# Optimization experiments

Hardware: AMD Instinct MI355X
Metric: run time of the kernel (lower is better)

Reference implementation:

```python
import jax, jax.numpy as jnp
import numpy as np

B, Q, D, H, DH = 4, 1024, 1024, 16, 64  # batch, qlen(=klen), d_model, n_head, d_head
SCALE = 1.0 / np.sqrt(DH)
_INF = -1e30
LN_EPS = 1e-5


def setup_inputs() -> dict:
    key = jax.random.key(0)
    ks = jax.random.split(key, 10)
    w = jax.random.normal(ks[0], (B, Q, D), jnp.float32)
    r = jax.random.normal(ks[1], (Q, D), jnp.float32)
    r_w_bias = jax.random.normal(ks[2], (H, DH), jnp.float32) * 0.02
    r_r_bias = jax.random.normal(ks[3], (H, DH), jnp.float32) * 0.02
    # causal mask: nonzero = attend (torch masks where attn_mask == 0)
    attn_mask = jnp.tile(jnp.tril(jnp.ones((Q, Q), bool))[None], (B, 1, 1))
    # linear weights stored torch-style: (out_features, in_features), no bias
    Wq = jax.random.normal(ks[4], (H * DH, D), jnp.float32) * SCALE
    Wk = jax.random.normal(ks[5], (H * DH, D), jnp.float32) * SCALE
    Wv = jax.random.normal(ks[6], (H * DH, D), jnp.float32) * SCALE
    Wo = jax.random.normal(ks[7], (D, H * DH), jnp.float32) * SCALE
    Wr = jax.random.normal(ks[8], (H * DH, D), jnp.float32) * (1.0 / np.sqrt(H * DH))
    ln_gamma = jnp.ones((D,), jnp.float32)
    ln_beta = jnp.zeros((D,), jnp.float32)
    return {"w": w, "r": r, "r_w_bias": r_w_bias, "r_r_bias": r_r_bias,
            "attn_mask": attn_mask, "Wq": Wq, "Wk": Wk, "Wv": Wv, "Wr": Wr,
            "Wo": Wo, "ln_gamma": ln_gamma, "ln_beta": ln_beta}


def _layer_norm(x, gamma, beta):
    mu = jnp.mean(x, axis=-1, keepdims=True)
    var = jnp.mean(jnp.square(x - mu), axis=-1, keepdims=True)
    return (x - mu) * jax.lax.rsqrt(var + LN_EPS) * gamma + beta


def _rel_shift(x):
    # faithful to this repo: pad one zero column on key axis then drop first
    # column -> left-shift along j with trailing zeros (no reshape trick)
    return jnp.concatenate([x[:, :, 1:, :], jnp.zeros_like(x[:, :, :1, :])], axis=2)


def reference(w, r, r_w_bias, r_r_bias, attn_mask, Wq, Wk, Wv, Wr, Wo, ln_gamma, ln_beta):
    bsz, qlen, _ = w.shape
    klen = qlen  # no mems
    r_head_k = (r @ Wr.T).reshape(klen, H, DH)          # [K,H,Dh]
    w_head_q = (w @ Wq.T).reshape(bsz, qlen, H, DH)     # [B,Q,H,Dh]
    w_head_k = (w @ Wk.T).reshape(bsz, klen, H, DH)
    w_head_v = (w @ Wv.T).reshape(bsz, klen, H, DH)
    AC = jnp.einsum('bind,bjnd->bijn', w_head_q + r_w_bias, w_head_k)
    BD = jnp.einsum('bind,jnd->bijn', w_head_q + r_r_bias, r_head_k)
    BD = _rel_shift(BD)
    attn_score = (AC + BD) * SCALE                      # [B,Q,K,H]
    attn_score = jnp.where(attn_mask[..., None], attn_score, _INF)
    attn_prob = jax.nn.softmax(attn_score, axis=2)
    attn_vec = jnp.einsum('bijn,bjnd->bind', attn_prob, w_head_v)
    attn_vec = attn_vec.reshape(bsz, qlen, H * DH)
    attn_out = attn_vec @ Wo.T
    return _layer_norm(w + attn_out, ln_gamma, ln_beta)
```

## Files before the change

kernel.cpp:

```cpp
#include <hip/hip_runtime.h>
#include <math.h>

typedef _Float16 F16;
typedef __attribute__((ext_vector_type(8))) _Float16 f16x8;
typedef __attribute__((ext_vector_type(4))) float f32x4;

__global__ __launch_bounds__(256) void cvt_kernel(const float* __restrict__ src,
                                                  F16* __restrict__ dst, int n4) {
  int i = blockIdx.x * 256 + threadIdx.x;
  if (i >= n4) return;
  float4 v = reinterpret_cast<const float4*>(src)[i];
  union { F16 h[4]; uint2 u; } pk;
  pk.h[0] = (F16)v.x; pk.h[1] = (F16)v.y; pk.h[2] = (F16)v.z; pk.h[3] = (F16)v.w;
  reinterpret_cast<uint2*>(dst)[i] = pk.u;
}

__global__ void fill_kernel(F16* __restrict__ Kt) {
  int id = blockIdx.x * 256 + threadIdx.x;
  int b = id >> 10, h = (id >> 6) & 15, d = id & 63;
  Kt[(((size_t)(b * 16 + h)) * 1024 + 1023) * 128 + 64 + d] = (F16)0.f;
}

template <int MODE>
__global__ __launch_bounds__(256) void gemm_bt(const F16* __restrict__ A,
                                               const F16* __restrict__ W,
                                               const float* __restrict__ bias1,
                                               const float* __restrict__ bias2,
                                               F16* __restrict__ outp,
                                               float* __restrict__ outf,
                                               const float* __restrict__ addsrc) {
  const int tid = threadIdx.x;
  const int lane = tid & 63, wid = tid >> 6;
  const int wm = wid >> 1, wn = wid & 1;
  const int l15 = lane & 15, g = lane >> 4, hi8 = g * 8;
  const int m0 = blockIdx.x * 128, n0 = blockIdx.y * 128;

  __shared__ __align__(16) F16 As[128][72];
  __shared__ __align__(16) F16 Bs[128][72];

  f32x4 acc[4][4] = {};

  for (int k0 = 0; k0 < 1024; k0 += 64) {
#pragma unroll
    for (int j = 0; j < 4; ++j) {
      int chunk = tid + j * 256;
      int r = chunk >> 3, cc = (chunk & 7) * 8;
      *(uint4*)&As[r][cc] = *(const uint4*)&A[(size_t)(m0 + r) * 1024 + k0 + cc];
      *(uint4*)&Bs[r][cc] = *(const uint4*)&W[(size_t)(n0 + r) * 1024 + k0 + cc];
    }
    __syncthreads();
#pragma unroll
    for (int kk = 0; kk < 2; ++kk) {
      f16x8 a[4], b[4];
#pragma unroll
      for (int m = 0; m < 4; ++m) a[m] = *(const f16x8*)&As[wm * 64 + m * 16 + l15][kk * 32 + hi8];
#pragma unroll
      for (int n = 0; n < 4; ++n) b[n] = *(const f16x8*)&Bs[wn * 64 + n * 16 + l15][kk * 32 + hi8];
#pragma unroll
      for (int m = 0; m < 4; ++m)
#pragma unroll
        for (int n = 0; n < 4; ++n)
          acc[m][n] = __builtin_amdgcn_mfma_f32_16x16x32_f16(a[m], b[n], acc[m][n], 0, 0, 0);
    }
    __syncthreads();
  }

#pragma unroll
  for (int m = 0; m < 4; ++m)
#pragma unroll
    for (int n = 0; n < 4; ++n)
#pragma unroll
      for (int i = 0; i < 4; ++i) {
        int row = m0 + wm * 64 + m * 16 + g * 4 + i;
        int col = n0 + wn * 64 + n * 16 + l15;
        float v = acc[m][n][i];
        if (MODE == 0) {
          int b = row >> 10, q = row & 1023, h = col >> 6, d = col & 63;
          size_t base = (((size_t)(b * 16 + h)) * 1024 + q) * 128;
          outp[base + d]      = (F16)((v + bias1[col]) * 0.125f);
          outp[base + 64 + d] = (F16)((v + bias2[col]) * 0.125f);
        } else if (MODE == 1) {
          int b = row >> 10, q = row & 1023, h = col >> 6, d = col & 63;
          outp[(((size_t)(b * 16 + h)) * 1024 + q) * 128 + d] = (F16)v;
        } else if (MODE == 2) {
          int b = row >> 10, q = row & 1023, h = col >> 6, d = col & 63;
          outp[(((size_t)(b * 16 + h)) * 64 + d) * 1024 + q] = (F16)v;
        } else if (MODE == 3) {
          if (row > 0) {
            int h = col >> 6, d = col & 63;
#pragma unroll
            for (int b2 = 0; b2 < 4; ++b2)
              outp[(((size_t)(b2 * 16 + h)) * 1024 + (row - 1)) * 128 + 64 + d] = (F16)v;
          }
        } else {
          outf[(size_t)row * 1024 + col] = v + addsrc[(size_t)row * 1024 + col];
        }
      }
}

__global__ __launch_bounds__(256) void attn_kernel(const F16* __restrict__ Qt,
                                                   const F16* __restrict__ Kt,
                                                   const F16* __restrict__ Vt,
                                                   F16* __restrict__ av) {
  const int qb = blockIdx.x, h = blockIdx.y, b = blockIdx.z;
  const int tid = threadIdx.x, lane = tid & 63, w = tid >> 6;
  const int l15 = lane & 15, g = lane >> 4, hi8 = g * 8;
  const size_t bh = (size_t)(b * 16 + h);
  const F16* Qb = Qt + bh * 1024 * 128;
  const F16* Kb = Kt + bh * 1024 * 128;
  const F16* Vb = Vt + bh * 64 * 1024;

  __shared__ __align__(16) F16 Ks[64][136];
  __shared__ __align__(16) F16 Vs[64][72];
  __shared__ __align__(16) F16 Ps[4][16][72];

  f16x8 qf[4];
  const int qrow = qb * 64 + w * 16 + l15;
#pragma unroll
  for (int t = 0; t < 4; ++t)
    qf[t] = *(const f16x8*)&Qb[(size_t)qrow * 128 + t * 32 + hi8];

  f32x4 accO[4] = {};
  float mi[4], li[4];
#pragma unroll
  for (int i = 0; i < 4; ++i) { mi[i] = -INFINITY; li[i] = 0.f; }

  for (int kt = 0; kt <= qb; ++kt) {
#pragma unroll
    for (int j = 0; j < 4; ++j) {
      int chunk = tid + j * 256;
      int r = chunk >> 4, cc = (chunk & 15) * 8;
      *(uint4*)&Ks[r][cc] = *(const uint4*)&Kb[(size_t)(kt * 64 + r) * 128 + cc];
    }
#pragma unroll
    for (int j = 0; j < 2; ++j) {
      int chunk = tid + j * 256;
      int r = chunk >> 3, cc = (chunk & 7) * 8;
      *(uint4*)&Vs[r][cc] = *(const uint4*)&Vb[(size_t)r * 1024 + kt * 64 + cc];
    }
    __syncthreads();

    f32x4 s[4] = {};
#pragma unroll
    for (int st = 0; st < 4; ++st)
#pragma unroll
      for (int t = 0; t < 4; ++t) {
        f16x8 kf = *(const f16x8*)&Ks[st * 16 + l15][t * 32 + hi8];
        s[st] = __builtin_amdgcn_mfma_f32_16x16x32_f16(qf[t], kf, s[st], 0, 0, 0);
      }

    if (kt == qb) {
#pragma unroll
      for (int st = 0; st < 4; ++st)
#pragma unroll
        for (int i = 0; i < 4; ++i) {
          int row = qb * 64 + w * 16 + g * 4 + i;
          int col = kt * 64 + st * 16 + l15;
          if (col > row) s[st][i] = -1e30f;
        }
    }

#pragma unroll
    for (int i = 0; i < 4; ++i) {
      float v = fmaxf(fmaxf(s[0][i], s[1][i]), fmaxf(s[2][i], s[3][i]));
      v = fmaxf(v, __shfl_xor(v, 1));
      v = fmaxf(v, __shfl_xor(v, 2));
      v = fmaxf(v, __shfl_xor(v, 4));
      v = fmaxf(v, __shfl_xor(v, 8));
      float mnew = fmaxf(mi[i], v);
      float sum = 0.f;
#pragma unroll
      for (int st = 0; st < 4; ++st) {
        float p = __expf(s[st][i] - mnew);
        sum += p;
        Ps[w][g * 4 + i][st * 16 + l15] = (F16)p;
      }
      sum += __shfl_xor(sum, 1);
      sum += __shfl_xor(sum, 2);
      sum += __shfl_xor(sum, 4);
      sum += __shfl_xor(sum, 8);
      float alpha = __expf(mi[i] - mnew);
      li[i] = li[i] * alpha + sum;
      mi[i] = mnew;
#pragma unroll
      for (int n = 0; n < 4; ++n) accO[n][i] *= alpha;
    }

#pragma unroll
    for (int t2 = 0; t2 < 2; ++t2) {
      f16x8 pa = *(const f16x8*)&Ps[w][l15][t2 * 32 + hi8];
#pragma unroll
      for (int n = 0; n < 4; ++n) {
        f16x8 vb = *(const f16x8*)&Vs[n * 16 + l15][t2 * 32 + hi8];
        accO[n] = __builtin_amdgcn_mfma_f32_16x16x32_f16(pa, vb, accO[n], 0, 0, 0);
      }
    }
    __syncthreads();
  }

#pragma unroll
  for (int n = 0; n < 4; ++n)
#pragma unroll
    for (int i = 0; i < 4; ++i) {
      int row = qb * 64 + w * 16 + g * 4 + i;
      av[((size_t)b * 1024 + row) * 1024 + h * 64 + n * 16 + l15] =
          (F16)(accO[n][i] / li[i]);
    }
}

__global__ __launch_bounds__(256) void ln_kernel(const float* __restrict__ x,
                                                 const float* __restrict__ gamma,
                                                 const float* __restrict__ beta,
                                                 float* __restrict__ out) {
  const int row = blockIdx.x;
  const int t = threadIdx.x;
  const float* xr = x + (size_t)row * 1024;
  float4 v = reinterpret_cast<const float4*>(xr)[t];
  float s = v.x + v.y + v.z + v.w;
  float s2 = v.x * v.x + v.y * v.y + v.z * v.z + v.w * v.w;
  for (int off = 32; off; off >>= 1) {
    s += __shfl_down(s, off);
    s2 += __shfl_down(s2, off);
  }
  __shared__ float ps[4], ps2[4];
  int wid = t >> 6, ln = t & 63;
  if (ln == 0) { ps[wid] = s; ps2[wid] = s2; }
  __syncthreads();
  if (t == 0) {
    float a = 0, c = 0;
    for (int i = 0; i < 4; ++i) { a += ps[i]; c += ps2[i]; }
    ps[0] = a; ps2[0] = c;
  }
  __syncthreads();
  float mean = ps[0] * (1.f / 1024.f);
  float var = ps2[0] * (1.f / 1024.f) - mean * mean;
  float rstd = rsqrtf(var + 1e-5f);
  float4 gm = reinterpret_cast<const float4*>(gamma)[t];
  float4 bt = reinterpret_cast<const float4*>(beta)[t];
  float4 o;
  o.x = (v.x - mean) * rstd * gm.x + bt.x;
  o.y = (v.y - mean) * rstd * gm.y + bt.y;
  o.z = (v.z - mean) * rstd * gm.z + bt.z;
  o.w = (v.w - mean) * rstd * gm.w + bt.w;
  reinterpret_cast<float4*>(out + (size_t)row * 1024)[t] = o;
}

extern "C" void kernel_launch(void* const* d_in, const int* in_sizes, int n_in,
                              void* d_out, int out_size, void* d_ws, size_t ws_size,
                              hipStream_t stream) {
  const float* w = (const float*)d_in[0];
  const float* r = (const float*)d_in[1];
  const float* rwb = (const float*)d_in[2];
  const float* rrb = (const float*)d_in[3];
  const float* Wq = (const float*)d_in[5];
  const float* Wk = (const float*)d_in[6];
  const float* Wv = (const float*)d_in[7];
  const float* Wr = (const float*)d_in[8];
  const float* Wo = (const float*)d_in[9];
  const float* gamma = (const float*)d_in[10];
  const float* beta = (const float*)d_in[11];
  float* out = (float*)d_out;

  char* ws = (char*)d_ws;
  size_t off = 0;
  F16* w_bf = (F16*)(ws + off); off += (size_t)4096 * 1024 * 2;
  F16* r_bf = (F16*)(ws + off); off += (size_t)1024 * 1024 * 2;
  F16* wq_bf = (F16*)(ws + off); off += (size_t)1024 * 1024 * 2;
  F16* wk_bf = (F16*)(ws + off); off += (size_t)1024 * 1024 * 2;
  F16* wv_bf = (F16*)(ws + off); off += (size_t)1024 * 1024 * 2;
  F16* wr_bf = (F16*)(ws + off); off += (size_t)1024 * 1024 * 2;
  F16* wo_bf = (F16*)(ws + off); off += (size_t)1024 * 1024 * 2;
  F16* Qt = (F16*)(ws + off); off += (size_t)4 * 16 * 1024 * 128 * 2;
  F16* Kt = (F16*)(ws + off); off += (size_t)4 * 16 * 1024 * 128 * 2;
  F16* Vt = (F16*)(ws + off); off += (size_t)4 * 16 * 64 * 1024 * 2;
  F16* av = (F16*)(ws + off); off += (size_t)4096 * 1024 * 2;
  float* tmp = (float*)(ws + off); off += (size_t)4096 * 1024 * 4;

  cvt_kernel<<<4096, 256, 0, stream>>>(w, w_bf, 1048576);
  cvt_kernel<<<1024, 256, 0, stream>>>(r, r_bf, 262144);
  cvt_kernel<<<1024, 256, 0, stream>>>(Wq, wq_bf, 262144);
  cvt_kernel<<<1024, 256, 0, stream>>>(Wk, wk_bf, 262144);
  cvt_kernel<<<1024, 256, 0, stream>>>(Wv, wv_bf, 262144);
  cvt_kernel<<<1024, 256, 0, stream>>>(Wr, wr_bf, 262144);
  cvt_kernel<<<1024, 256, 0, stream>>>(Wo, wo_bf, 262144);
  fill_kernel<<<16, 256, 0, stream>>>(Kt);

  gemm_bt<0><<<dim3(32, 8), 256, 0, stream>>>(w_bf, wq_bf, rwb, rrb, Qt, nullptr, nullptr);
  gemm_bt<1><<<dim3(32, 8), 256, 0, stream>>>(w_bf, wk_bf, nullptr, nullptr, Kt, nullptr, nullptr);
  gemm_bt<2><<<dim3(32, 8), 256, 0, stream>>>(w_bf, wv_bf, nullptr, nullptr, Vt, nullptr, nullptr);
  gemm_bt<3><<<dim3(8, 8), 256, 0, stream>>>(r_bf, wr_bf, nullptr, nullptr, Kt, nullptr, nullptr);

  attn_kernel<<<dim3(16, 16, 4), 256, 0, stream>>>(Qt, Kt, Vt, av);

  gemm_bt<4><<<dim3(32, 8), 256, 0, stream>>>(av, wo_bf, nullptr, nullptr, nullptr, tmp, w);
  ln_kernel<<<4096, 256, 0, stream>>>(tmp, gamma, beta, out);
}
```

Measured before the change: 353.9 us.

## Fuse QKV projection GEMMs, pair causal attention tiles, double-buffer and swizzle K/V LDS

The Q, K and V weights are packed into one 3072-column matrix so a single GEMM launch with a widened grid produces all three outputs, each with its own epilogue layout. The attention kernel now has each block process a pair of query tiles (qt and 15-qt), which evens out the causal triangle's work across blocks and halves the grid. It also prefetches the next K/V tile into registers while computing the current one, writes into double-buffered LDS, and uses an XOR swizzle instead of padding to avoid bank conflicts. In exchange it adds an extra barrier per iteration and more register pressure.

```diff
diff --git a/kernel.cpp b/kernel.cpp
--- a/kernel.cpp
+++ b/kernel.cpp
@@ -26,7 +26,9 @@
                                                const F16* __restrict__ W,
                                                const float* __restrict__ bias1,
                                                const float* __restrict__ bias2,
-                                               F16* __restrict__ outp,
+                                               F16* __restrict__ outq,
+                                               F16* __restrict__ outk,
+                                               F16* __restrict__ outv,
                                                float* __restrict__ outf,
                                                const float* __restrict__ addsrc) {
   const int tid = threadIdx.x;
@@ -75,22 +77,24 @@
         int col = n0 + wn * 64 + n * 16 + l15;
         float v = acc[m][n][i];
         if (MODE == 0) {
-          int b = row >> 10, q = row & 1023, h = col >> 6, d = col & 63;
-          size_t base = (((size_t)(b * 16 + h)) * 1024 + q) * 128;
-          outp[base + d]      = (F16)((v + bias1[col]) * 0.125f);
-          outp[base + 64 + d] = (F16)((v + bias2[col]) * 0.125f);
-        } else if (MODE == 1) {
-          int b = row >> 10, q = row & 1023, h = col >> 6, d = col & 63;
-          outp[(((size_t)(b * 16 + h)) * 1024 + q) * 128 + d] = (F16)v;
-        } else if (MODE == 2) {
-          int b = row >> 10, q = row & 1023, h = col >> 6, d = col & 63;
-          outp[(((size_t)(b * 16 + h)) * 64 + d) * 1024 + q] = (F16)v;
+          int which = col >> 10, c = col & 1023;
+          int hh = c >> 6, d = c & 63;
+          int bb = row >> 10, q = row & 1023;
+          if (which == 0) {
+            size_t base = (((size_t)(bb * 16 + hh)) * 1024 + q) * 128;
+            outq[base + d]      = (F16)((v + bias1[c]) * 0.125f);
+            outq[base + 64 + d] = (F16)((v + bias2[c]) * 0.125f);
+          } else if (which == 1) {
+            outk[(((size_t)(bb * 16 + hh)) * 1024 + q) * 128 + d] = (F16)v;
+          } else {
+            outv[(((size_t)(bb * 16 + hh)) * 64 + d) * 1024 + q] = (F16)v;
+          }
         } else if (MODE == 3) {
           if (row > 0) {
-            int h = col >> 6, d = col & 63;
+            int hh = col >> 6, d = col & 63;
 #pragma unroll
             for (int b2 = 0; b2 < 4; ++b2)
-              outp[(((size_t)(b2 * 16 + h)) * 1024 + (row - 1)) * 128 + 64 + d] = (F16)v;
+              outk[(((size_t)(b2 * 16 + hh)) * 1024 + (row - 1)) * 128 + 64 + d] = (F16)v;
           }
         } else {
           outf[(size_t)row * 1024 + col] = v + addsrc[(size_t)row * 1024 + col];
@@ -102,62 +106,86 @@
                                                    const F16* __restrict__ Kt,
                                                    const F16* __restrict__ Vt,
                                                    F16* __restrict__ av) {
-  const int qb = blockIdx.x, h = blockIdx.y, b = blockIdx.z;
+  const int qpair = blockIdx.x, h = blockIdx.y, b = blockIdx.z;
   const int tid = threadIdx.x, lane = tid & 63, w = tid >> 6;
   const int l15 = lane & 15, g = lane >> 4, hi8 = g * 8;
   const size_t bh = (size_t)(b * 16 + h);
   const F16* Qb = Qt + bh * 1024 * 128;
   const F16* Kb = Kt + bh * 1024 * 128;
   const F16* Vb = Vt + bh * 64 * 1024;
-
-  __shared__ __align__(16) F16 Ks[64][136];
-  __shared__ __align__(16) F16 Vs[64][72];
+  const int qt0 = qpair, qt1 = 15 - qpair;
+  const int nit = qt0 + qt1 + 2;
+
+  __shared__ __align__(16) F16 Ks[2][64][128];
+  __shared__ __align__(16) F16 Vs[2][64][64];
   __shared__ __align__(16) F16 Ps[4][16][72];
 
+  const int kr0 = tid >> 4, kc0 = tid & 15;
+  const int vr0 = tid >> 3, vc0 = tid & 7;
+
+  uint4 kreg[4], vreg[2];
+
+  auto kt_of = [&](int it) { return it <= qt0 ? it : it - qt0 - 1; };
+
+  auto load_regs = [&](int it) {
+    int kt = kt_of(it);
+#pragma unroll
+    for (int j = 0; j < 4; ++j)
+      kreg[j] = *(const uint4*)&Kb[(size_t)(kt * 64 + kr0 + j * 16) * 128 + kc0 * 8];
+#pragma unroll
+    for (int j = 0; j < 2; ++j)
+      vreg[j] = *(const uint4*)&Vb[(size_t)(vr0 + j * 32) * 1024 + kt * 64 + vc0 * 8];
+  };
+  auto write_regs = [&](int buf) {
+#pragma unroll
+    for (int j = 0; j < 4; ++j) {
+      int r = kr0 + j * 16;
+      *(uint4*)&Ks[buf][r][(kc0 ^ (r & 7)) * 8] = kreg[j];
+    }
+#pragma unroll
+    for (int j = 0; j < 2; ++j) {
+      int r = vr0 + j * 32;
+      *(uint4*)&Vs[buf][r][(vc0 ^ (r & 7)) * 8] = vreg[j];
+    }
+  };
+
+  int qtile = qt0;
+  int qrow = qtile * 64 + w * 16 + l15;
   f16x8 qf[4];
-  const int qrow = qb * 64 + w * 16 + l15;
-#pragma unroll
-  for (int t = 0; t < 4; ++t)
-    qf[t] = *(const f16x8*)&Qb[(size_t)qrow * 128 + t * 32 + hi8];
+#pragma unroll
+  for (int t = 0; t < 4; ++t) qf[t] = *(const f16x8*)&Qb[(size_t)qrow * 128 + t * 32 + hi8];
 
   f32x4 accO[4] = {};
   float mi[4], li[4];
 #pragma unroll
   for (int i = 0; i < 4; ++i) { mi[i] = -INFINITY; li[i] = 0.f; }
 
-  for (int kt = 0; kt <= qb; ++kt) {
-#pragma unroll
-    for (int j = 0; j < 4; ++j) {
-      int chunk = tid + j * 256;
-      int r = chunk >> 4, cc = (chunk & 15) * 8;
-      *(uint4*)&Ks[r][cc] = *(const uint4*)&Kb[(size_t)(kt * 64 + r) * 128 + cc];
-    }
-#pragma unroll
-    for (int j = 0; j < 2; ++j) {
-      int chunk = tid + j * 256;
-      int r = chunk >> 3, cc = (chunk & 7) * 8;
-      *(uint4*)&Vs[r][cc] = *(const uint4*)&Vb[(size_t)r * 1024 + kt * 64 + cc];
-    }
-    __syncthreads();
+  load_regs(0);
+  write_regs(0);
+  __syncthreads();
+
+  for (int it = 0; it < nit; ++it) {
+    const int buf = it & 1;
+    const int kt = kt_of(it);
+    if (it + 1 < nit) load_regs(it + 1);
 
     f32x4 s[4] = {};
 #pragma unroll
-    for (int st = 0; st < 4; ++st)
+    for (int st = 0; st < 4; ++st) {
+      const int krow = st * 16 + l15, swz = krow & 7;
 #pragma unroll
       for (int t = 0; t < 4; ++t) {
-        f16x8 kf = *(const f16x8*)&Ks[st * 16 + l15][t * 32 + hi8];
+        f16x8 kf = *(const f16x8*)&Ks[buf][krow][((t * 4 + g) ^ swz) * 8];
         s[st] = __builtin_amdgcn_mfma_f32_16x16x32_f16(qf[t], kf, s[st], 0, 0, 0);
       }
-
-    if (kt == qb) {
+    }
+
+    if (kt == qtile) {
 #pragma unroll
       for (int st = 0; st < 4; ++st)
 #pragma unroll
-        for (int i = 0; i < 4; ++i) {
-          int row = qb * 64 + w * 16 + g * 4 + i;
-          int col = kt * 64 + st * 16 + l15;
-          if (col > row) s[st][i] = -1e30f;
-        }
+        for (int i = 0; i < 4; ++i)
+          if (st * 16 + l15 > w * 16 + g * 4 + i) s[st][i] = -1e30f;
     }
 
 #pragma unroll
@@ -191,21 +219,38 @@
       f16x8 pa = *(const f16x8*)&Ps[w][l15][t2 * 32 + hi8];
 #pragma unroll
       for (int n = 0; n < 4; ++n) {
-        f16x8 vb = *(const f16x8*)&Vs[n * 16 + l15][t2 * 32 + hi8];
+        const int vrow = n * 16 + l15;
+        f16x8 vb = *(const f16x8*)&Vs[buf][vrow][((t2 * 4 + g) ^ (vrow & 7)) * 8];
         accO[n] = __builtin_amdgcn_mfma_f32_16x16x32_f16(pa, vb, accO[n], 0, 0, 0);
       }
     }
+
+    if (kt == qtile) {
+#pragma unroll
+      for (int n = 0; n < 4; ++n)
+#pragma unroll
+        for (int i = 0; i < 4; ++i) {
+          int row = qtile * 64 + w * 16 + g * 4 + i;
+          av[((size_t)b * 1024 + row) * 1024 + h * 64 + n * 16 + l15] =
+              (F16)(accO[n][i] / li[i]);
+        }
+      if (it + 1 < nit) {
+        qtile = qt1;
+        qrow = qtile * 64 + w * 16 + l15;
+#pragma unroll
+        for (int t = 0; t < 4; ++t)
+          qf[t] = *(const f16x8*)&Qb[(size_t)qrow * 128 + t * 32 + hi8];
+#pragma unroll
+        for (int i = 0; i < 4; ++i) { mi[i] = -INFINITY; li[i] = 0.f; }
+#pragma unroll
+        for (int n = 0; n < 4; ++n) accO[n] = f32x4{0.f, 0.f, 0.f, 0.f};
+      }
+    }
+
+    __syncthreads();
+    if (it + 1 < nit) write_regs(buf ^ 1);
     __syncthreads();
   }
-
-#pragma unroll
-  for (int n = 0; n < 4; ++n)
-#pragma unroll
-    for (int i = 0; i < 4; ++i) {
-      int row = qb * 64 + w * 16 + g * 4 + i;
-      av[((size_t)b * 1024 + row) * 1024 + h * 64 + n * 16 + l15] =
-          (F16)(accO[n][i] / li[i]);
-    }
 }
 
 __global__ __launch_bounds__(256) void ln_kernel(const float* __restrict__ x,
@@ -263,35 +308,31 @@
 
   char* ws = (char*)d_ws;
   size_t off = 0;
-  F16* w_bf = (F16*)(ws + off); off += (size_t)4096 * 1024 * 2;
-  F16* r_bf = (F16*)(ws + off); off += (size_t)1024 * 1024 * 2;
-  F16* wq_bf = (F16*)(ws + off); off += (size_t)1024 * 1024 * 2;
-  F16* wk_bf = (F16*)(ws + off); off += (size_t)1024 * 1024 * 2;
-  F16* wv_bf = (F16*)(ws + off); off += (size_t)1024 * 1024 * 2;
-  F16* wr_bf = (F16*)(ws + off); off += (size_t)1024 * 1024 * 2;
-  F16* wo_bf = (F16*)(ws + off); off += (size_t)1024 * 1024 * 2;
+  F16* w_f = (F16*)(ws + off); off += (size_t)4096 * 1024 * 2;
+  F16* r_f = (F16*)(ws + off); off += (size_t)1024 * 1024 * 2;
+  F16* wqkv_f = (F16*)(ws + off); off += (size_t)3 * 1024 * 1024 * 2;
+  F16* wr_f = (F16*)(ws + off); off += (size_t)1024 * 1024 * 2;
+  F16* wo_f = (F16*)(ws + off); off += (size_t)1024 * 1024 * 2;
   F16* Qt = (F16*)(ws + off); off += (size_t)4 * 16 * 1024 * 128 * 2;
   F16* Kt = (F16*)(ws + off); off += (size_t)4 * 16 * 1024 * 128 * 2;
   F16* Vt = (F16*)(ws + off); off += (size_t)4 * 16 * 64 * 1024 * 2;
   F16* av = (F16*)(ws + off); off += (size_t)4096 * 1024 * 2;
   float* tmp = (float*)(ws + off); off += (size_t)4096 * 1024 * 4;
 
-  cvt_kernel<<<4096, 256, 0, stream>>>(w, w_bf, 1048576);
-  cvt_kernel<<<1024, 256, 0, stream>>>(r, r_bf, 262144);
-  cvt_kernel<<<1024, 256, 0, stream>>>(Wq, wq_bf, 262144);
-  cvt_kernel<<<1024, 256, 0, stream>>>(Wk, wk_bf, 262144);
-  cvt_kernel<<<1024, 256, 0, stream>>>(Wv, wv_bf, 262144);
-  cvt_kernel<<<1024, 256, 0, stream>>>(Wr, wr_bf, 262144);
-  cvt_kernel<<<1024, 256, 0, stream>>>(Wo, wo_bf, 262144);
+  cvt_kernel<<<4096, 256, 0, stream>>>(w, w_f, 1048576);
+  cvt_kernel<<<1024, 256, 0, stream>>>(r, r_f, 262144);
+  cvt_kernel<<<1024, 256, 0, stream>>>(Wq, wqkv_f, 262144);
+  cvt_kernel<<<1024, 256, 0, stream>>>(Wk, wqkv_f + (size_t)1024 * 1024, 262144);
+  cvt_kernel<<<1024, 256, 0, stream>>>(Wv, wqkv_f + (size_t)2 * 1024 * 1024, 262144);
+  cvt_kernel<<<1024, 256, 0, stream>>>(Wr, wr_f, 262144);
+  cvt_kernel<<<1024, 256, 0, stream>>>(Wo, wo_f, 262144);
   fill_kernel<<<16, 256, 0, stream>>>(Kt);
 
-  gemm_bt<0><<<dim3(32, 8), 256, 0, stream>>>(w_bf, wq_bf, rwb, rrb, Qt, nullptr, nullptr);
-  gemm_bt<1><<<dim3(32, 8), 256, 0, stream>>>(w_bf, wk_bf, nullptr, nullptr, Kt, nullptr, nullptr);
-  gemm_bt<2><<<dim3(32, 8), 256, 0, stream>>>(w_bf, wv_bf, nullptr, nullptr, Vt, nullptr, nullptr);
-  gemm_bt<3><<<dim3(8, 8), 256, 0, stream>>>(r_bf, wr_bf, nullptr, nullptr, Kt, nullptr, nullptr);
-
-  attn_kernel<<<dim3(16, 16, 4), 256, 0, stream>>>(Qt, Kt, Vt, av);
-
-  gemm_bt<4><<<dim3(32, 8), 256, 0, stream>>>(av, wo_bf, nullptr, nullptr, nullptr, tmp, w);
+  gemm_bt<0><<<dim3(32, 24), 256, 0, stream>>>(w_f, wqkv_f, rwb, rrb, Qt, Kt, Vt, nullptr, nullptr);
+  gemm_bt<3><<<dim3(8, 8), 256, 0, stream>>>(r_f, wr_f, nullptr, nullptr, nullptr, Kt, nullptr, nullptr, nullptr);
+
+  attn_kernel<<<dim3(8, 16, 4), 256, 0, stream>>>(Qt, Kt, Vt, av);
+
+  gemm_bt<4><<<dim3(32, 8), 256, 0, stream>>>(av, wo_f, nullptr, nullptr, nullptr, nullptr, nullptr, tmp, w);
   ln_kernel<<<4096, 256, 0, stream>>>(tmp, gamma, beta, out);
 }
```

New measurement: 308.8 us. 1.15x faster.
